# Performance work log

Measured on AMD Instinct MI355X. Metric: run time of the kernel, lower is better.

## Reference

```python
import jax, jax.numpy as jnp
import numpy as np

N = 100000   # points in input set
K = 1024     # num centroids AND max neighbors per ball (as in original code)
C = 64       # input feature channels
R = 0.2      # ball radius
LAYERS = (64, 64, 128)


def setup_inputs() -> dict:
    key = jax.random.key(0)
    ks = jax.random.split(key, 9)
    coords = jax.random.uniform(ks[0], (N, 3), dtype=jnp.float32)
    features = jax.random.normal(ks[1], (N, C), dtype=jnp.float32)
    centroid_idx = jax.random.randint(ks[2], (K,), 0, N)
    dims = (3 + C,) + LAYERS
    params = {}
    for i in range(len(LAYERS)):
        fin, fout = dims[i], dims[i + 1]
        params[f"W{i+1}"] = (jax.random.normal(ks[3 + i], (fin, fout), dtype=jnp.float32)
                             / np.float32(np.sqrt(fin)))
        params[f"b{i+1}"] = jax.random.normal(ks[6 + i], (fout,), dtype=jnp.float32) * 0.01
    return dict(coords=coords, features=features, centroid_idx=centroid_idx, **params)


def reference(coords, features, centroid_idx, W1, b1, W2, b2, W3, b3):
    cent = coords[centroid_idx]                                   # [K,3]
    # squared distances [K,N] without materializing [K,N,3]
    d2 = (jnp.sum(cent * cent, axis=-1)[:, None]
          + jnp.sum(coords * coords, axis=-1)[None, :]
          - 2.0 * cent @ coords.T)
    mask = d2 <= R * R                                            # ball query
    # take the FIRST K in-radius points in original index order (matches [:K])
    rank = jnp.cumsum(mask.astype(jnp.int32), axis=1) - 1
    sel = mask & (rank < K)
    order = jnp.where(sel, jnp.arange(N)[None, :], N)
    idx = jnp.sort(order, axis=1)[:, :K]                          # [K,K]
    valid = idx < N
    idx_c = jnp.minimum(idx, N - 1)
    rel = coords[idx_c] - cent[:, None, :]                        # centered coords
    x = jnp.concatenate([rel, features[idx_c]], axis=-1)          # [K,K,3+C]
    for W, b in ((W1, b1), (W2, b2), (W3, b3)):
        x = jax.nn.relu(x @ W + b)
    x = jnp.where(valid[:, :, None], x, -jnp.inf)
    new_features = jnp.max(x, axis=1)                             # per-region max pool
    return cent, new_features
```

## Files before the change

### kernel.cpp

```cpp
#include <hip/hip_runtime.h>
#include <hip/hip_bf16.h>

#define NPTS    100000
#define KCENT   1024
#define NSEG    391
#define NWORDS  1564
#define WSTRIDE 1600
#define MB_BLKS (NSEG*32)

typedef __attribute__((ext_vector_type(8))) short bf16x8;
typedef __attribute__((ext_vector_type(4))) float f32x4;
typedef unsigned long long u64;

__device__ __forceinline__ unsigned short f2bf(float x) {
  union { float f; unsigned u; } v; v.f = x;
  unsigned r = v.u + 0x7FFFu + ((v.u >> 16) & 1u);
  return (unsigned short)(r >> 16);
}
__device__ __forceinline__ unsigned pk2bf(float a, float b) {
  union { __hip_bfloat162 h; unsigned u; } cv;
  cv.h = __float22bfloat162_rn(make_float2(a, b));
  return cv.u;
}
__device__ __forceinline__ bf16x8 pack_bf8(f32x4 a, f32x4 b) {
  union { bf16x8 v; unsigned u[4]; } r;
  r.u[0] = pk2bf(a[0], a[1]); r.u[1] = pk2bf(a[2], a[3]);
  r.u[2] = pk2bf(b[0], b[1]); r.u[3] = pk2bf(b[2], b[3]);
  return r.v;
}

__global__ __launch_bounds__(256) void build_prep_kernel(
    const float* __restrict__ coords, const float* __restrict__ features,
    const int* __restrict__ cidx, const float* __restrict__ W1,
    const float* __restrict__ b1, const float* __restrict__ W2,
    const float* __restrict__ W3, u64* __restrict__ maskbuf,
    unsigned short* __restrict__ featsBF, f32x4* __restrict__ coords4,
    unsigned short* __restrict__ W1T, unsigned short* __restrict__ W2T,
    unsigned short* __restrict__ W3T, float* __restrict__ outCent) {
  const int bid = blockIdx.x;
  const int tid = threadIdx.x;
  if (bid < MB_BLKS) {
    const int grp = bid / NSEG, seg = bid - grp*NSEG;
    __shared__ float sC[96];
    __shared__ float sCC[32];
    if (tid < 96) sC[tid] = coords[cidx[grp*32 + tid/3]*3 + tid%3];
    __syncthreads();
    if (tid < 32) {
      float x = sC[tid*3], y = sC[tid*3+1], z = sC[tid*3+2];
      sCC[tid] = __fadd_rn(__fadd_rn(__fmul_rn(x,x), __fmul_rn(y,y)), __fmul_rn(z,z));
    }
    const int p = seg*256 + tid;
    const bool inr = p < NPTS;
    float px = 0.f, py = 0.f, pz = 0.f;
    if (inr) { px = coords[p*3]; py = coords[p*3+1]; pz = coords[p*3+2]; }
    const float pp = __fadd_rn(__fadd_rn(__fmul_rn(px,px), __fmul_rn(py,py)), __fmul_rn(pz,pz));
    __syncthreads();
    const int lane = tid & 63, wid = tid >> 6;
    u64 myw = 0ull;
    #pragma unroll
    for (int ci = 0; ci < 32; ++ci) {
      float cx = sC[ci*3], cy = sC[ci*3+1], cz = sC[ci*3+2];
      float dt = __fadd_rn(__fadd_rn(__fmul_rn(cx,px), __fmul_rn(cy,py)), __fmul_rn(cz,pz));
      float d2 = __fsub_rn(__fadd_rn(sCC[ci], pp), __fmul_rn(2.0f, dt));
      bool sel = inr && (d2 <= 0.04f);
      u64 m = __ballot(sel);
      if (lane == ci) myw = m;
    }
    if (lane < 32)
      maskbuf[(u64)(grp*32 + lane)*WSTRIDE + seg*4 + wid] = myw;
    return;
  }
  int i = (bid - MB_BLKS) * 256 + tid;
  if (i < 800000) {
    const f32x4* src = (const f32x4*)features + i*2;
    f32x4 f0 = src[0], f1 = src[1];
    union { bf16x8 v; uint4 u; } pk; pk.v = pack_bf8(f0, f1);
    ((uint4*)featsBF)[i] = pk.u;
    return;
  }
  i -= 800000;
  if (i < NPTS) {
    coords4[i] = (f32x4){coords[3*i], coords[3*i+1], coords[3*i+2], 0.f};
    return;
  }
  i -= NPTS;
  if (i < 6144) {
    int n = i / 96, kk = i - n*96;
    float v = 0.f;
    if (kk < 64)       v = W1[(3+kk)*64 + n];
    else if (kk < 67)  v = W1[(kk-64)*64 + n];
    else if (kk == 67) v = b1[n];
    W1T[n*104 + kk] = f2bf(v);
    return;
  }
  i -= 6144;
  if (i < 4608) { int n = i / 72, kk = i - n*72;
    W2T[n*72 + kk] = f2bf(kk < 64 ? W2[kk*64 + n] : 0.f); return; }
  i -= 4608;
  if (i < 9216) { int n = i / 72, kk = i - n*72;
    W3T[n*72 + kk] = f2bf(kk < 64 ? W3[kk*128 + n] : 0.f); return; }
  i -= 9216;
  if (i < KCENT) {
    int ci = cidx[i];
    outCent[i*3+0] = coords[ci*3+0];
    outCent[i*3+1] = coords[ci*3+1];
    outCent[i*3+2] = coords[ci*3+2];
  }
}

__global__ __launch_bounds__(256) void maskemit_kernel(
    const u64* __restrict__ maskbuf, int* __restrict__ idxbuf,
    int* __restrict__ counts) {
  __shared__ int sTot[4];
  const int c = blockIdx.x;
  const int tid = threadIdx.x;
  const int lane = tid & 63, w = tid >> 6;
  const u64* M = maskbuf + (u64)c * WSTRIDE;
  int* out = idxbuf + (c << 10);
  u64 wv[7];
  #pragma unroll
  for (int r = 0; r < 7; ++r) {
    int widx = r*256 + tid;
    wv[r] = (widx < NWORDS) ? M[widx] : 0ull;
  }
  int base = 0;
  #pragma unroll 1
  for (int r = 0; r < 7; ++r) {
    u64 word = wv[r];
    int pc = __popcll(word);
    int inc = pc;
    #pragma unroll
    for (int d = 1; d < 64; d <<= 1) {
      int t = __shfl_up(inc, d);
      if (lane >= d) inc += t;
    }
    if (lane == 63) sTot[w] = inc;
    __syncthreads();
    int wbase = 0, tot = 0;
    #pragma unroll
    for (int i = 0; i < 4; ++i) { int v = sTot[i]; tot += v; if (i < w) wbase += v; }
    int pos = base + wbase + inc - pc;
    const int pbase = (r*256 + tid) * 64;
    while (word != 0ull && pos < KCENT) {
      int b = __ffsll(word) - 1;
      out[pos++] = pbase + b;
      word &= word - 1ull;
    }
    base += tot;
    __syncthreads();
    if (base >= KCENT) break;
  }
  if (tid == 0) counts[c] = base < KCENT ? base : KCENT;
}

__global__ __launch_bounds__(256, 3) void fused_kernel(
    const unsigned short* __restrict__ featsBF, const f32x4* __restrict__ coords4,
    const float* __restrict__ cent, const int* __restrict__ idxbuf,
    const int* __restrict__ counts, const float* __restrict__ b2v,
    const unsigned short* __restrict__ gW1T, const unsigned short* __restrict__ gW2T,
    const unsigned short* __restrict__ gW3T, float* __restrict__ pmax) {
  __shared__ __align__(16) unsigned short sW1T[64*104];
  __shared__ __align__(16) unsigned short sW2T[64*72];
  __shared__ __align__(16) unsigned short sW3T[128*72];
  __shared__ __align__(16) unsigned short sH[4*2*16*72];
  __shared__ float sB2[64];
  __shared__ float sMax[512];

  const int bx = blockIdx.x;
  const int k = bx >> 1, b = bx & 1;
  const int tid = threadIdx.x;
  const int w = tid >> 6, lane = tid & 63;
  const int q = lane >> 4, cl = lane & 15;

  for (int i = tid; i < 832; i += 256)  ((uint4*)sW1T)[i] = ((const uint4*)gW1T)[i];
  for (int i = tid; i < 576; i += 256)  ((uint4*)sW2T)[i] = ((const uint4*)gW2T)[i];
  for (int i = tid; i < 1152; i += 256) ((uint4*)sW3T)[i] = ((const uint4*)gW3T)[i];
  if (tid < 64) sB2[tid] = b2v[tid];

  const int count = counts[k];
  const float cx = cent[k*3], cy = cent[k*3+1], cz = cent[k*3+2];
  unsigned short* myHA = sH + w*2304;
  unsigned short* myHB = myHA + 1152;
  const int kb = k << 10;
  __syncthreads();

  f32x4 runmax[8];
  #pragma unroll
  for (int i = 0; i < 8; ++i)
    runmax[i] = (f32x4){-__builtin_inff(), -__builtin_inff(),
                        -__builtin_inff(), -__builtin_inff()};

  const int nstrips = (count + 15) >> 4;
  const int npairs  = (nstrips + 1) >> 1;
  int pp = 2*w + b;

  int pA = 0, pB = 0;
  { int jA = 32*pp + cl;      if (jA < count) pA = idxbuf[kb + jA];
    int jB = 32*pp + 16 + cl; if (jB < count) pB = idxbuf[kb + jB]; }
  f32x4  c4A = coords4[pA], c4B = coords4[pB];
  bf16x8 xfA0 = *(const bf16x8*)(featsBF + pA*64 + q*8);
  bf16x8 xfA1 = *(const bf16x8*)(featsBF + pA*64 + 32 + q*8);
  bf16x8 xfB0 = *(const bf16x8*)(featsBF + pB*64 + q*8);
  bf16x8 xfB1 = *(const bf16x8*)(featsBF + pB*64 + 32 + q*8);
  int pA2 = 0, pB2 = 0;
  { int jA = 32*(pp+8) + cl;      if (jA < count) pA2 = idxbuf[kb + jA];
    int jB = 32*(pp+8) + 16 + cl; if (jB < count) pB2 = idxbuf[kb + jB]; }

  const bf16x8 zero8 = (bf16x8){0,0,0,0,0,0,0,0};

  for (; pp < npairs; pp += 8) {
    int pA3 = 0, pB3 = 0;
    { int jA = 32*(pp+16) + cl;      if (jA < count) pA3 = idxbuf[kb + jA];
      int jB = 32*(pp+16) + 16 + cl; if (jB < count) pB3 = idxbuf[kb + jB]; }

    union { bf16x8 v; unsigned u[4]; } rfA, rfB;
    rfA.u[0] = pk2bf(c4A[0]-cx, c4A[1]-cy); rfA.u[1] = pk2bf(c4A[2]-cz, 1.0f);
    rfA.u[2] = 0u; rfA.u[3] = 0u;
    rfB.u[0] = pk2bf(c4B[0]-cx, c4B[1]-cy); rfB.u[1] = pk2bf(c4B[2]-cz, 1.0f);
    rfB.u[2] = 0u; rfB.u[3] = 0u;
    bf16x8 x2A = (q == 0) ? rfA.v : zero8;
    bf16x8 x2B = (q == 0) ? rfB.v : zero8;

    {
      f32x4 accA[4], accB[4];
      #pragma unroll
      for (int nt = 0; nt < 4; ++nt) { accA[nt] = (f32x4){0.f,0.f,0.f,0.f};
                                       accB[nt] = (f32x4){0.f,0.f,0.f,0.f}; }
      #pragma unroll
      for (int nt = 0; nt < 4; ++nt) {
        const unsigned short* wrow = sW1T + (nt*16+cl)*104 + q*8;
        bf16x8 wa0 = *(const bf16x8*)(wrow);
        accA[nt] = __builtin_amdgcn_mfma_f32_16x16x32_bf16(wa0, xfA0, accA[nt], 0,0,0);
        accB[nt] = __builtin_amdgcn_mfma_f32_16x16x32_bf16(wa0, xfB0, accB[nt], 0,0,0);
        bf16x8 wa1 = *(const bf16x8*)(wrow + 32);
        accA[nt] = __builtin_amdgcn_mfma_f32_16x16x32_bf16(wa1, xfA1, accA[nt], 0,0,0);
        accB[nt] = __builtin_amdgcn_mfma_f32_16x16x32_bf16(wa1, xfB1, accB[nt], 0,0,0);
        bf16x8 wa2 = *(const bf16x8*)(wrow + 64);
        accA[nt] = __builtin_amdgcn_mfma_f32_16x16x32_bf16(wa2, x2A, accA[nt], 0,0,0);
        accB[nt] = __builtin_amdgcn_mfma_f32_16x16x32_bf16(wa2, x2B, accB[nt], 0,0,0);
      }
      #pragma unroll
      for (int nt = 0; nt < 4; ++nt) {
        const int o = nt*16 + q*4;
        uint2 pkA = { pk2bf(fmaxf(accA[nt][0],0.f), fmaxf(accA[nt][1],0.f)),
                      pk2bf(fmaxf(accA[nt][2],0.f), fmaxf(accA[nt][3],0.f)) };
        *(uint2*)(myHA + cl*72 + o) = pkA;
        uint2 pkB = { pk2bf(fmaxf(accB[nt][0],0.f), fmaxf(accB[nt][1],0.f)),
                      pk2bf(fmaxf(accB[nt][2],0.f), fmaxf(accB[nt][3],0.f)) };
        *(uint2*)(myHB + cl*72 + o) = pkB;
      }
    }

    c4A = coords4[pA2]; c4B = coords4[pB2];
    xfA0 = *(const bf16x8*)(featsBF + pA2*64 + q*8);
    xfA1 = *(const bf16x8*)(featsBF + pA2*64 + 32 + q*8);
    xfB0 = *(const bf16x8*)(featsBF + pB2*64 + q*8);
    xfB1 = *(const bf16x8*)(featsBF + pB2*64 + 32 + q*8);

    {
      bf16x8 hA0 = *(const bf16x8*)(myHA + cl*72 + q*8);
      bf16x8 hA1 = *(const bf16x8*)(myHA + cl*72 + 32 + q*8);
      bf16x8 hB0 = *(const bf16x8*)(myHB + cl*72 + q*8);
      bf16x8 hB1 = *(const bf16x8*)(myHB + cl*72 + 32 + q*8);
      f32x4 accA[4], accB[4];
      #pragma unroll
      for (int nt = 0; nt < 4; ++nt) { accA[nt] = (f32x4){0.f,0.f,0.f,0.f};
                                       accB[nt] = (f32x4){0.f,0.f,0.f,0.f}; }
      #pragma unroll
      for (int nt = 0; nt < 4; ++nt) {
        const unsigned short* wrow = sW2T + (nt*16+cl)*72 + q*8;
        bf16x8 wa0 = *(const bf16x8*)(wrow);
        accA[nt] = __builtin_amdgcn_mfma_f32_16x16x32_bf16(wa0, hA0, accA[nt], 0,0,0);
        accB[nt] = __builtin_amdgcn_mfma_f32_16x16x32_bf16(wa0, hB0, accB[nt], 0,0,0);
        bf16x8 wa1 = *(const bf16x8*)(wrow + 32);
        accA[nt] = __builtin_amdgcn_mfma_f32_16x16x32_bf16(wa1, hA1, accA[nt], 0,0,0);
        accB[nt] = __builtin_amdgcn_mfma_f32_16x16x32_bf16(wa1, hB1, accB[nt], 0,0,0);
      }
      #pragma unroll
      for (int nt = 0; nt < 4; ++nt) {
        const int o = nt*16 + q*4;
        f32x4 bb = *(const f32x4*)(sB2 + o);
        uint2 pkA = { pk2bf(fmaxf(accA[nt][0]+bb[0],0.f), fmaxf(accA[nt][1]+bb[1],0.f)),
                      pk2bf(fmaxf(accA[nt][2]+bb[2],0.f), fmaxf(accA[nt][3]+bb[3],0.f)) };
        *(uint2*)(myHA + cl*72 + o) = pkA;
        uint2 pkB = { pk2bf(fmaxf(accB[nt][0]+bb[0],0.f), fmaxf(accB[nt][1]+bb[1],0.f)),
                      pk2bf(fmaxf(accB[nt][2]+bb[2],0.f), fmaxf(accB[nt][3]+bb[3],0.f)) };
        *(uint2*)(myHB + cl*72 + o) = pkB;
      }
    }

    {
      bf16x8 hA0 = *(const bf16x8*)(myHA + cl*72 + q*8);
      bf16x8 hA1 = *(const bf16x8*)(myHA + cl*72 + 32 + q*8);
      bf16x8 hB0 = *(const bf16x8*)(myHB + cl*72 + q*8);
      bf16x8 hB1 = *(const bf16x8*)(myHB + cl*72 + 32 + q*8);
      const float vmA = (32*pp + cl      < count) ? 0.f : -__builtin_inff();
      const float vmB = (32*pp + 16 + cl < count) ? 0.f : -__builtin_inff();
      #pragma unroll
      for (int ntq = 0; ntq < 4; ++ntq) {
        f32x4 a3A[2], a3B[2];
        #pragma unroll
        for (int j = 0; j < 2; ++j) { a3A[j] = (f32x4){0.f,0.f,0.f,0.f};
                                      a3B[j] = (f32x4){0.f,0.f,0.f,0.f}; }
        #pragma unroll
        for (int j = 0; j < 2; ++j) {
          const int nt = ntq*2 + j;
          const unsigned short* wrow = sW3T + (nt*16+cl)*72 + q*8;
          bf16x8 w30 = *(const bf16x8*)(wrow);
          a3A[j] = __builtin_amdgcn_mfma_f32_16x16x32_bf16(w30, hA0, a3A[j], 0,0,0);
          a3B[j] = __builtin_amdgcn_mfma_f32_16x16x32_bf16(w30, hB0, a3B[j], 0,0,0);
          bf16x8 w31 = *(const bf16x8*)(wrow + 32);
          a3A[j] = __builtin_amdgcn_mfma_f32_16x16x32_bf16(w31, hA1, a3A[j], 0,0,0);
          a3B[j] = __builtin_amdgcn_mfma_f32_16x16x32_bf16(w31, hB1, a3B[j], 0,0,0);
        }
        #pragma unroll
        for (int j = 0; j < 2; ++j) {
          const int nt = ntq*2 + j;
          #pragma unroll
          for (int r = 0; r < 4; ++r)
            runmax[nt][r] = fmaxf(runmax[nt][r],
                                  fmaxf(a3A[j][r] + vmA, a3B[j][r] + vmB));
        }
      }
    }

    pA2 = pA3; pB2 = pB3;
  }

  #pragma unroll
  for (int nt = 0; nt < 8; ++nt) {
    #pragma unroll
    for (int r = 0; r < 4; ++r) {
      float m = runmax[nt][r];
      m = fmaxf(m, __shfl_xor(m, 1));
      m = fmaxf(m, __shfl_xor(m, 2));
      m = fmaxf(m, __shfl_xor(m, 4));
      m = fmaxf(m, __shfl_xor(m, 8));
      runmax[nt][r] = m;
    }
    if (cl == 0) *(f32x4*)(sMax + w*128 + nt*16 + q*4) = runmax[nt];
  }
  __syncthreads();
  if (tid < 128) {
    float m = fmaxf(fmaxf(sMax[tid], sMax[128+tid]),
                    fmaxf(sMax[256+tid], sMax[384+tid]));
    pmax[bx*128 + tid] = m;
  }
}

__global__ __launch_bounds__(256) void combine_kernel(
    const float* __restrict__ pmax, const float* __restrict__ b3,
    float* __restrict__ outF) {
  int i = blockIdx.x*256 + threadIdx.x;
  int kk = i >> 7, c = i & 127;
  float m = fmaxf(pmax[(2*kk)*128 + c], pmax[(2*kk+1)*128 + c]);
  outF[i] = fmaxf(m + b3[c], 0.f);
}

extern "C" void kernel_launch(void* const* d_in, const int* in_sizes, int n_in,
                              void* d_out, int out_size, void* d_ws, size_t ws_size,
                              hipStream_t stream) {
  const float* coords   = (const float*)d_in[0];
  const float* features = (const float*)d_in[1];
  const int*   cidx     = (const int*)d_in[2];
  const float* W1 = (const float*)d_in[3];
  const float* b1 = (const float*)d_in[4];
  const float* W2 = (const float*)d_in[5];
  const float* b2 = (const float*)d_in[6];
  const float* W3 = (const float*)d_in[7];
  const float* b3 = (const float*)d_in[8];
  float* out = (float*)d_out;

  char* ws = (char*)d_ws;
  u64* maskbuf            = (u64*)(ws + 0);
  unsigned short* featsBF = (unsigned short*)(ws + 13107200);
  f32x4* coords4          = (f32x4*)(ws + 25907200);
  int* idxbuf  = (int*)(ws + 27507200);
  int* counts  = (int*)(ws + 31701504);
  unsigned short* W1T = (unsigned short*)(ws + 31705600);
  unsigned short* W2T = (unsigned short*)(ws + 31718912);
  unsigned short* W3T = (unsigned short*)(ws + 31728128);
  float* pmax = (float*)(ws + 31746560);

  build_prep_kernel<<<MB_BLKS + 3598, 256, 0, stream>>>(
      coords, features, cidx, W1, b1, W2, W3,
      maskbuf, featsBF, coords4, W1T, W2T, W3T, out);
  maskemit_kernel<<<KCENT, 256, 0, stream>>>(maskbuf, idxbuf, counts);
  fused_kernel<<<2048, 256, 0, stream>>>(featsBF, coords4, out, idxbuf, counts,
                                         b2, W1T, W2T, W3T, pmax);
  combine_kernel<<<512, 256, 0, stream>>>(pmax, b3, out + 3072);
}
```

Baseline: 243.6 us.

## Fuse mask compaction, MLP and combine into one kernel per centroid

Merges the mask-to-index compaction kernel, the MLP/maxpool kernel and the combine kernel into a single kernel with one block per centroid. Neighbor indices now stay in shared memory instead of a global index buffer, and the b3 bias plus ReLU are applied in that kernel's epilogue. W1 and W3 fragments are kept in registers rather than re-read from LDS, and the layer-3 MFMAs run over all 8 output tiles at once. This removes two launches and the global round trip of idxbuf, counts and pmax. In exchange each block does twice as much MLP work with half as many blocks, and register pressure rises (launch bounds go from 3 to 2 blocks per CU), which may limit latency hiding.

```diff
diff --git a/kernel.cpp b/kernel.cpp
--- a/kernel.cpp
+++ b/kernel.cpp
@@ -90,7 +90,7 @@
     if (kk < 64)       v = W1[(3+kk)*64 + n];
     else if (kk < 67)  v = W1[(kk-64)*64 + n];
     else if (kk == 67) v = b1[n];
-    W1T[n*104 + kk] = f2bf(v);
+    W1T[n*96 + kk] = f2bf(v);
     return;
   }
   i -= 6144;
@@ -108,25 +108,49 @@
   }
 }
 
-__global__ __launch_bounds__(256) void maskemit_kernel(
-    const u64* __restrict__ maskbuf, int* __restrict__ idxbuf,
-    int* __restrict__ counts) {
+__global__ __launch_bounds__(256, 2) void fused_kernel(
+    const u64* __restrict__ maskbuf, const unsigned short* __restrict__ featsBF,
+    const f32x4* __restrict__ coords4, const float* __restrict__ cent,
+    const float* __restrict__ b2v, const float* __restrict__ b3v,
+    const unsigned short* __restrict__ gW1T, const unsigned short* __restrict__ gW2T,
+    const unsigned short* __restrict__ gW3T, float* __restrict__ outF) {
+  __shared__ __align__(16) unsigned short sW2T[64*72];
+  __shared__ __align__(16) unsigned short sH[4*2*16*72];
+  __shared__ int sIdx[KCENT];
   __shared__ int sTot[4];
-  const int c = blockIdx.x;
+  __shared__ float sB2[64], sB3[128];
+  __shared__ float sMax[512];
+
+  const int k = blockIdx.x;
   const int tid = threadIdx.x;
-  const int lane = tid & 63, w = tid >> 6;
-  const u64* M = maskbuf + (u64)c * WSTRIDE;
-  int* out = idxbuf + (c << 10);
-  u64 wv[7];
+  const int w = tid >> 6, lane = tid & 63;
+  const int q = lane >> 4, cl = lane & 15;
+
+  const u64* M = maskbuf + (u64)k * WSTRIDE;
+  u64 wv0 = M[tid], wv1 = M[256 + tid], wv2 = M[512 + tid];
+
+  for (int i = tid; i < 576; i += 256) ((uint4*)sW2T)[i] = ((const uint4*)gW2T)[i];
+  if (tid < 64)  sB2[tid] = b2v[tid];
+  if (tid < 128) sB3[tid] = b3v[tid];
+
+  bf16x8 w1f[3][4], w3f[2][8];
   #pragma unroll
-  for (int r = 0; r < 7; ++r) {
-    int widx = r*256 + tid;
-    wv[r] = (widx < NWORDS) ? M[widx] : 0ull;
-  }
+  for (int ks = 0; ks < 3; ++ks)
+    #pragma unroll
+    for (int nt = 0; nt < 4; ++nt)
+      w1f[ks][nt] = *(const bf16x8*)(gW1T + (nt*16+cl)*96 + ks*32 + q*8);
+  #pragma unroll
+  for (int ks = 0; ks < 2; ++ks)
+    #pragma unroll
+    for (int nt = 0; nt < 8; ++nt)
+      w3f[ks][nt] = *(const bf16x8*)(gW3T + (nt*16+cl)*72 + ks*32 + q*8);
+
   int base = 0;
   #pragma unroll 1
   for (int r = 0; r < 7; ++r) {
-    u64 word = wv[r];
+    const int widx = r*256 + tid;
+    u64 word = (r == 0) ? wv0 : (r == 1) ? wv1 : (r == 2) ? wv2
+             : ((widx < NWORDS) ? M[widx] : 0ull);
     int pc = __popcll(word);
     int inc = pc;
     #pragma unroll
@@ -140,49 +164,21 @@
     #pragma unroll
     for (int i = 0; i < 4; ++i) { int v = sTot[i]; tot += v; if (i < w) wbase += v; }
     int pos = base + wbase + inc - pc;
-    const int pbase = (r*256 + tid) * 64;
+    const int pbase = widx * 64;
     while (word != 0ull && pos < KCENT) {
       int b = __ffsll(word) - 1;
-      out[pos++] = pbase + b;
+      sIdx[pos++] = pbase + b;
       word &= word - 1ull;
     }
     base += tot;
     __syncthreads();
     if (base >= KCENT) break;
   }
-  if (tid == 0) counts[c] = base < KCENT ? base : KCENT;
-}
-
-__global__ __launch_bounds__(256, 3) void fused_kernel(
-    const unsigned short* __restrict__ featsBF, const f32x4* __restrict__ coords4,
-    const float* __restrict__ cent, const int* __restrict__ idxbuf,
-    const int* __restrict__ counts, const float* __restrict__ b2v,
-    const unsigned short* __restrict__ gW1T, const unsigned short* __restrict__ gW2T,
-    const unsigned short* __restrict__ gW3T, float* __restrict__ pmax) {
-  __shared__ __align__(16) unsigned short sW1T[64*104];
-  __shared__ __align__(16) unsigned short sW2T[64*72];
-  __shared__ __align__(16) unsigned short sW3T[128*72];
-  __shared__ __align__(16) unsigned short sH[4*2*16*72];
-  __shared__ float sB2[64];
-  __shared__ float sMax[512];
-
-  const int bx = blockIdx.x;
-  const int k = bx >> 1, b = bx & 1;
-  const int tid = threadIdx.x;
-  const int w = tid >> 6, lane = tid & 63;
-  const int q = lane >> 4, cl = lane & 15;
-
-  for (int i = tid; i < 832; i += 256)  ((uint4*)sW1T)[i] = ((const uint4*)gW1T)[i];
-  for (int i = tid; i < 576; i += 256)  ((uint4*)sW2T)[i] = ((const uint4*)gW2T)[i];
-  for (int i = tid; i < 1152; i += 256) ((uint4*)sW3T)[i] = ((const uint4*)gW3T)[i];
-  if (tid < 64) sB2[tid] = b2v[tid];
-
-  const int count = counts[k];
+  const int count = base < KCENT ? base : KCENT;
+
   const float cx = cent[k*3], cy = cent[k*3+1], cz = cent[k*3+2];
   unsigned short* myHA = sH + w*2304;
   unsigned short* myHB = myHA + 1152;
-  const int kb = k << 10;
-  __syncthreads();
 
   f32x4 runmax[8];
   #pragma unroll
@@ -192,26 +188,26 @@
 
   const int nstrips = (count + 15) >> 4;
   const int npairs  = (nstrips + 1) >> 1;
-  int pp = 2*w + b;
+  int pp = w;
 
   int pA = 0, pB = 0;
-  { int jA = 32*pp + cl;      if (jA < count) pA = idxbuf[kb + jA];
-    int jB = 32*pp + 16 + cl; if (jB < count) pB = idxbuf[kb + jB]; }
+  { int jA = 32*pp + cl;      if (jA < count) pA = sIdx[jA];
+    int jB = 32*pp + 16 + cl; if (jB < count) pB = sIdx[jB]; }
   f32x4  c4A = coords4[pA], c4B = coords4[pB];
   bf16x8 xfA0 = *(const bf16x8*)(featsBF + pA*64 + q*8);
   bf16x8 xfA1 = *(const bf16x8*)(featsBF + pA*64 + 32 + q*8);
   bf16x8 xfB0 = *(const bf16x8*)(featsBF + pB*64 + q*8);
   bf16x8 xfB1 = *(const bf16x8*)(featsBF + pB*64 + 32 + q*8);
   int pA2 = 0, pB2 = 0;
-  { int jA = 32*(pp+8) + cl;      if (jA < count) pA2 = idxbuf[kb + jA];
-    int jB = 32*(pp+8) + 16 + cl; if (jB < count) pB2 = idxbuf[kb + jB]; }
+  { int jA = 32*(pp+4) + cl;      if (jA < count) pA2 = sIdx[jA];
+    int jB = 32*(pp+4) + 16 + cl; if (jB < count) pB2 = sIdx[jB]; }
 
   const bf16x8 zero8 = (bf16x8){0,0,0,0,0,0,0,0};
 
-  for (; pp < npairs; pp += 8) {
+  for (; pp < npairs; pp += 4) {
     int pA3 = 0, pB3 = 0;
-    { int jA = 32*(pp+16) + cl;      if (jA < count) pA3 = idxbuf[kb + jA];
-      int jB = 32*(pp+16) + 16 + cl; if (jB < count) pB3 = idxbuf[kb + jB]; }
+    { int jA = 32*(pp+8) + cl;      if (jA < count) pA3 = sIdx[jA];
+      int jB = 32*(pp+8) + 16 + cl; if (jB < count) pB3 = sIdx[jB]; }
 
     union { bf16x8 v; unsigned u[4]; } rfA, rfB;
     rfA.u[0] = pk2bf(c4A[0]-cx, c4A[1]-cy); rfA.u[1] = pk2bf(c4A[2]-cz, 1.0f);
@@ -228,16 +224,18 @@
                                        accB[nt] = (f32x4){0.f,0.f,0.f,0.f}; }
       #pragma unroll
       for (int nt = 0; nt < 4; ++nt) {
-        const unsigned short* wrow = sW1T + (nt*16+cl)*104 + q*8;
-        bf16x8 wa0 = *(const bf16x8*)(wrow);
-        accA[nt] = __builtin_amdgcn_mfma_f32_16x16x32_bf16(wa0, xfA0, accA[nt], 0,0,0);
-        accB[nt] = __builtin_amdgcn_mfma_f32_16x16x32_bf16(wa0, xfB0, accB[nt], 0,0,0);
-        bf16x8 wa1 = *(const bf16x8*)(wrow + 32);
-        accA[nt] = __builtin_amdgcn_mfma_f32_16x16x32_bf16(wa1, xfA1, accA[nt], 0,0,0);
-        accB[nt] = __builtin_amdgcn_mfma_f32_16x16x32_bf16(wa1, xfB1, accB[nt], 0,0,0);
-        bf16x8 wa2 = *(const bf16x8*)(wrow + 64);
-        accA[nt] = __builtin_amdgcn_mfma_f32_16x16x32_bf16(wa2, x2A, accA[nt], 0,0,0);
-        accB[nt] = __builtin_amdgcn_mfma_f32_16x16x32_bf16(wa2, x2B, accB[nt], 0,0,0);
+        accA[nt] = __builtin_amdgcn_mfma_f32_16x16x32_bf16(w1f[0][nt], xfA0, accA[nt], 0,0,0);
+        accB[nt] = __builtin_amdgcn_mfma_f32_16x16x32_bf16(w1f[0][nt], xfB0, accB[nt], 0,0,0);
+      }
+      #pragma unroll
+      for (int nt = 0; nt < 4; ++nt) {
+        accA[nt] = __builtin_amdgcn_mfma_f32_16x16x32_bf16(w1f[1][nt], xfA1, accA[nt], 0,0,0);
+        accB[nt] = __builtin_amdgcn_mfma_f32_16x16x32_bf16(w1f[1][nt], xfB1, accB[nt], 0,0,0);
+      }
+      #pragma unroll
+      for (int nt = 0; nt < 4; ++nt) {
+        accA[nt] = __builtin_amdgcn_mfma_f32_16x16x32_bf16(w1f[2][nt], x2A, accA[nt], 0,0,0);
+        accB[nt] = __builtin_amdgcn_mfma_f32_16x16x32_bf16(w1f[2][nt], x2B, accB[nt], 0,0,0);
       }
       #pragma unroll
       for (int nt = 0; nt < 4; ++nt) {
@@ -296,32 +294,26 @@
       bf16x8 hB1 = *(const bf16x8*)(myHB + cl*72 + 32 + q*8);
       const float vmA = (32*pp + cl      < count) ? 0.f : -__builtin_inff();
       const float vmB = (32*pp + 16 + cl < count) ? 0.f : -__builtin_inff();
-      #pragma unroll
-      for (int ntq = 0; ntq < 4; ++ntq) {
-        f32x4 a3A[2], a3B[2];
+      f32x4 a3A[8], a3B[8];
+      #pragma unroll
+      for (int nt = 0; nt < 8; ++nt) { a3A[nt] = (f32x4){0.f,0.f,0.f,0.f};
+                                       a3B[nt] = (f32x4){0.f,0.f,0.f,0.f}; }
+      #pragma unroll
+      for (int nt = 0; nt < 8; ++nt) {
+        a3A[nt] = __builtin_amdgcn_mfma_f32_16x16x32_bf16(w3f[0][nt], hA0, a3A[nt], 0,0,0);
+        a3B[nt] = __builtin_amdgcn_mfma_f32_16x16x32_bf16(w3f[0][nt], hB0, a3B[nt], 0,0,0);
+      }
+      #pragma unroll
+      for (int nt = 0; nt < 8; ++nt) {
+        a3A[nt] = __builtin_amdgcn_mfma_f32_16x16x32_bf16(w3f[1][nt], hA1, a3A[nt], 0,0,0);
+        a3B[nt] = __builtin_amdgcn_mfma_f32_16x16x32_bf16(w3f[1][nt], hB1, a3B[nt], 0,0,0);
+      }
+      #pragma unroll
+      for (int nt = 0; nt < 8; ++nt)
         #pragma unroll
-        for (int j = 0; j < 2; ++j) { a3A[j] = (f32x4){0.f,0.f,0.f,0.f};
-                                      a3B[j] = (f32x4){0.f,0.f,0.f,0.f}; }
-        #pragma unroll
-        for (int j = 0; j < 2; ++j) {
-          const int nt = ntq*2 + j;
-          const unsigned short* wrow = sW3T + (nt*16+cl)*72 + q*8;
-          bf16x8 w30 = *(const bf16x8*)(wrow);
-          a3A[j] = __builtin_amdgcn_mfma_f32_16x16x32_bf16(w30, hA0, a3A[j], 0,0,0);
-          a3B[j] = __builtin_amdgcn_mfma_f32_16x16x32_bf16(w30, hB0, a3B[j], 0,0,0);
-          bf16x8 w31 = *(const bf16x8*)(wrow + 32);
-          a3A[j] = __builtin_amdgcn_mfma_f32_16x16x32_bf16(w31, hA1, a3A[j], 0,0,0);
-          a3B[j] = __builtin_amdgcn_mfma_f32_16x16x32_bf16(w31, hB1, a3B[j], 0,0,0);
-        }
-        #pragma unroll
-        for (int j = 0; j < 2; ++j) {
-          const int nt = ntq*2 + j;
-          #pragma unroll
-          for (int r = 0; r < 4; ++r)
-            runmax[nt][r] = fmaxf(runmax[nt][r],
-                                  fmaxf(a3A[j][r] + vmA, a3B[j][r] + vmB));
-        }
-      }
+        for (int r = 0; r < 4; ++r)
+          runmax[nt][r] = fmaxf(runmax[nt][r],
+                                fmaxf(a3A[nt][r] + vmA, a3B[nt][r] + vmB));
     }
 
     pA2 = pA3; pB2 = pB3;
@@ -344,17 +336,8 @@
   if (tid < 128) {
     float m = fmaxf(fmaxf(sMax[tid], sMax[128+tid]),
                     fmaxf(sMax[256+tid], sMax[384+tid]));
-    pmax[bx*128 + tid] = m;
-  }
-}
-
-__global__ __launch_bounds__(256) void combine_kernel(
-    const float* __restrict__ pmax, const float* __restrict__ b3,
-    float* __restrict__ outF) {
-  int i = blockIdx.x*256 + threadIdx.x;
-  int kk = i >> 7, c = i & 127;
-  float m = fmaxf(pmax[(2*kk)*128 + c], pmax[(2*kk+1)*128 + c]);
-  outF[i] = fmaxf(m + b3[c], 0.f);
+    outF[k*128 + tid] = fmaxf(m + sB3[tid], 0.f);
+  }
 }
 
 extern "C" void kernel_launch(void* const* d_in, const int* in_sizes, int n_in,
@@ -375,18 +358,14 @@
   u64* maskbuf            = (u64*)(ws + 0);
   unsigned short* featsBF = (unsigned short*)(ws + 13107200);
   f32x4* coords4          = (f32x4*)(ws + 25907200);
-  int* idxbuf  = (int*)(ws + 27507200);
-  int* counts  = (int*)(ws + 31701504);
-  unsigned short* W1T = (unsigned short*)(ws + 31705600);
-  unsigned short* W2T = (unsigned short*)(ws + 31718912);
-  unsigned short* W3T = (unsigned short*)(ws + 31728128);
-  float* pmax = (float*)(ws + 31746560);
+  unsigned short* W1T = (unsigned short*)(ws + 27507200);
+  unsigned short* W2T = (unsigned short*)(ws + 27519488);
+  unsigned short* W3T = (unsigned short*)(ws + 27528704);
 
   build_prep_kernel<<<MB_BLKS + 3598, 256, 0, stream>>>(
       coords, features, cidx, W1, b1, W2, W3,
       maskbuf, featsBF, coords4, W1T, W2T, W3T, out);
-  maskemit_kernel<<<KCENT, 256, 0, stream>>>(maskbuf, idxbuf, counts);
-  fused_kernel<<<2048, 256, 0, stream>>>(featsBF, coords4, out, idxbuf, counts,
-                                         b2, W1T, W2T, W3T, pmax);
-  combine_kernel<<<512, 256, 0, stream>>>(pmax, b3, out + 3072);
-}
+  fused_kernel<<<KCENT, 256, 0, stream>>>(
+      maskbuf, featsBF, coords4, out, b2, b3,
+      W1T, W2T, W3T, out + 3072);
+}
```

Result: faster. 219.4 us (-9.9%).
